# Optimization experiments

Measured on AMD Instinct MI355X. Metric: run time of the kernel, lower is better.

## Reference

```python
import jax, jax.numpy as jnp
import numpy as np

T, B, I, H = 8192, 1, 1024, 1024


def _lstm_layer(x, W_ih, W_hh, b_ih, b_hh):
    # x: [T, B, I]; torch gate order: input, forget, cell(g), output
    Hh = W_hh.shape[1]
    xg = jnp.einsum('tbi,gi->tbg', x, W_ih) + b_ih + b_hh  # [T, B, 4H]

    def step(carry, xg_t):
        h, c = carry
        gates = xg_t + h @ W_hh.T  # [B, 4H]
        i, f, g, o = jnp.split(gates, 4, axis=-1)
        c = jax.nn.sigmoid(f) * c + jax.nn.sigmoid(i) * jnp.tanh(g)
        h = jax.nn.sigmoid(o) * jnp.tanh(c)
        return (h, c), h

    h0 = jnp.zeros((x.shape[1], Hh), x.dtype)
    (_, _), ys = jax.lax.scan(step, (h0, h0), xg)
    return ys  # [T, B, H]


def setup_inputs() -> dict:
    key = jax.random.key(0)
    ks = jax.random.split(key, 9)
    s = 0.02
    return {
        'inputs': jax.random.normal(ks[0], (T, B, I), dtype=jnp.float32),
        'W_ih0': jax.random.normal(ks[1], (4 * H, I), dtype=jnp.float32) * s,
        'W_hh0': jax.random.normal(ks[2], (4 * H, H), dtype=jnp.float32) * s,
        'b_ih0': jax.random.normal(ks[3], (4 * H,), dtype=jnp.float32) * s,
        'b_hh0': jax.random.normal(ks[4], (4 * H,), dtype=jnp.float32) * s,
        'W_ih1': jax.random.normal(ks[5], (4 * H, H), dtype=jnp.float32) * s,
        'W_hh1': jax.random.normal(ks[6], (4 * H, H), dtype=jnp.float32) * s,
        'b_ih1': jax.random.normal(ks[7], (4 * H,), dtype=jnp.float32) * s,
        'b_hh1': jax.random.normal(ks[8], (4 * H,), dtype=jnp.float32) * s,
    }


def reference(inputs, W_ih0, W_hh0, b_ih0, b_hh0, W_ih1, W_hh1, b_ih1, b_hh1):
    # 2-layer LSTM, zero initial state, dropout omitted (eval semantics)
    y0 = _lstm_layer(inputs, W_ih0, W_hh0, b_ih0, b_hh0)
    y1 = _lstm_layer(y0, W_ih1, W_hh1, b_ih1, b_hh1)
    return y1[-1]  # [B, H] — last timestep of top layer
```

## Files before the change

kernel.cpp:

```cpp
#include <hip/hip_runtime.h>

#define T_STEPS 8192
#define HID 1024
#define G4 4096
#define NBLK 128
#define NTHR 512
#define NSLOT 8

typedef unsigned int uint32;

struct Comm {
    uint32 hA[NSLOT][HID];
    uint32 hB[NSLOT][HID];
};

#define LD_AG  __HIP_MEMORY_SCOPE_AGENT

__device__ inline float sigm(float x) { return 1.0f / (1.0f + __expf(-x)); }
__device__ inline float tanh_f(float x) {
    x = fminf(fmaxf(x, -15.f), 15.f);
    float e = __expf(-2.0f * x);
    return (1.0f - e) / (1.0f + e);
}
__device__ inline uint32 tagf(float f, uint32 tg) {
    union { float f; uint32 u; } a; a.f = f;
    return (a.u & ~15u) | tg;
}

__global__ __launch_bounds__(256)
void gemm_xg(const float* __restrict__ A, const float* __restrict__ W,
             const float* __restrict__ bi, const float* __restrict__ bh,
             float* __restrict__ out)
{
    __shared__ float As[16][65];
    __shared__ float Bs[16][65];
    const int tid = threadIdx.x;
    const int m0 = blockIdx.y * 64, n0 = blockIdx.x * 64;
    const int tm = tid & 15, tn = tid >> 4;
    const int row = tid >> 2, q = tid & 3;
    float acc[4][4] = {{0.f}};
    for (int k0 = 0; k0 < HID; k0 += 16) {
        float4 a = *(const float4*)(A + (size_t)(m0 + row) * HID + k0 + q * 4);
        float4 b = *(const float4*)(W + (size_t)(n0 + row) * HID + k0 + q * 4);
        __syncthreads();
        As[q*4+0][row] = a.x; As[q*4+1][row] = a.y; As[q*4+2][row] = a.z; As[q*4+3][row] = a.w;
        Bs[q*4+0][row] = b.x; Bs[q*4+1][row] = b.y; Bs[q*4+2][row] = b.z; Bs[q*4+3][row] = b.w;
        __syncthreads();
#pragma unroll
        for (int kk = 0; kk < 16; ++kk) {
            float av[4], bv[4];
#pragma unroll
            for (int i = 0; i < 4; ++i) { av[i] = As[kk][tm*4+i]; bv[i] = Bs[kk][tn*4+i]; }
#pragma unroll
            for (int i = 0; i < 4; ++i)
#pragma unroll
                for (int j = 0; j < 4; ++j) acc[i][j] += av[i] * bv[j];
        }
    }
#pragma unroll
    for (int i = 0; i < 4; ++i) {
        int m = m0 + tm * 4 + i;
#pragma unroll
        for (int j = 0; j < 4; ++j) {
            int n = n0 + tn * 4 + j;
            float v = acc[i][j] + bi[n] + bh[n];
            int jd = n & (HID - 1), gate = n >> 10;
            out[(size_t)m * G4 + (jd >> 3) * 32 + (jd & 7) * 4 + gate] = v;
        }
    }
}

__device__ __forceinline__ void red4(float& a0, float& a1, float& a2, float& a3)
{
#pragma unroll
    for (int off = 32; off > 0; off >>= 1) {
        a0 += __shfl_xor(a0, off, 64);
        a1 += __shfl_xor(a1, off, 64);
        a2 += __shfl_xor(a2, off, 64);
        a3 += __shfl_xor(a3, off, 64);
    }
}

__device__ __forceinline__ void poll_gather(const uint32* __restrict__ buf, uint32 tg,
                                            int lane, float* __restrict__ lds)
{
    const uint32* p = buf + lane * 4;
    uint4 v0, v1, v2, v3;
    unsigned done = 0;
    for (;;) {
        if (!(done & 1u)) asm volatile("global_load_dwordx4 %0, %1, off sc0 sc1"             : "=v"(v0) : "v"(p) : "memory");
        if (!(done & 2u)) asm volatile("global_load_dwordx4 %0, %1, off offset:1024 sc0 sc1" : "=v"(v1) : "v"(p) : "memory");
        if (!(done & 4u)) asm volatile("global_load_dwordx4 %0, %1, off offset:2048 sc0 sc1" : "=v"(v2) : "v"(p) : "memory");
        if (!(done & 8u)) asm volatile("global_load_dwordx4 %0, %1, off offset:3072 sc0 sc1" : "=v"(v3) : "v"(p) : "memory");
        asm volatile("s_waitcnt vmcnt(0)" ::: "memory");
        __builtin_amdgcn_sched_barrier(0);
        if (!(done & 1u) && (v0.x & 15u) == tg && (v0.y & 15u) == tg &&
            (v0.z & 15u) == tg && (v0.w & 15u) == tg) done |= 1u;
        if (!(done & 2u) && (v1.x & 15u) == tg && (v1.y & 15u) == tg &&
            (v1.z & 15u) == tg && (v1.w & 15u) == tg) done |= 2u;
        if (!(done & 4u) && (v2.x & 15u) == tg && (v2.y & 15u) == tg &&
            (v2.z & 15u) == tg && (v2.w & 15u) == tg) done |= 4u;
        if (!(done & 8u) && (v3.x & 15u) == tg && (v3.y & 15u) == tg &&
            (v3.z & 15u) == tg && (v3.w & 15u) == tg) done |= 8u;
        if (__all(done == 15u)) break;
        __builtin_amdgcn_s_sleep(1);
    }
    union { uint4 u; float4 f; } c;
    c.u = v0; ((float4*)lds)[  0 + lane] = c.f;
    c.u = v1; ((float4*)lds)[ 64 + lane] = c.f;
    c.u = v2; ((float4*)lds)[128 + lane] = c.f;
    c.u = v3; ((float4*)lds)[192 + lane] = c.f;
}

__global__ __launch_bounds__(NTHR)
void lstm_fused(const float* __restrict__ Whh0, const float* __restrict__ xg,
                const float* __restrict__ Wih1, const float* __restrict__ Whh1,
                const float* __restrict__ bih1, const float* __restrict__ bhh1,
                float* __restrict__ outF, Comm* __restrict__ cm)
{
    __shared__ float hlA[2][HID];
    __shared__ float hlB[2][HID];
    const int tid = threadIdx.x;
    const int wave = tid >> 6, lane = tid & 63;
    const int kb = blockIdx.x;
    const int j = 8 * kb + wave;

    float whh0[4][16], whh1[4][16], wih1[4][16];
#pragma unroll
    for (int g = 0; g < 4; ++g) {
        const float* p0 = Whh0 + (size_t)(g * HID + j) * HID + lane;
        const float* p1 = Whh1 + (size_t)(g * HID + j) * HID + lane;
        const float* p2 = Wih1 + (size_t)(g * HID + j) * HID + lane;
#pragma unroll
        for (int u = 0; u < 16; ++u) {
            whh0[g][u] = p0[u * 64];
            whh1[g][u] = p1[u * 64];
            wih1[g][u] = p2[u * 64];
        }
    }
    float bia[4];
#pragma unroll
    for (int g = 0; g < 4; ++g) bia[g] = bih1[g * HID + j] + bhh1[g * HID + j];

    for (int i = tid; i < HID; i += NTHR) {
        hlA[0][i] = 0.f; hlA[1][i] = 0.f; hlB[0][i] = 0.f; hlB[1][i] = 0.f;
    }

    float c0 = 0.f, c1 = 0.f;
    float nx0 = 0.f, nx1 = 0.f, nx2 = 0.f, nx3 = 0.f;
    if (lane == 0) {
        const float* xp = xg + kb * 32 + wave * 4;
        nx0 = xp[0]; nx1 = xp[1]; nx2 = xp[2]; nx3 = xp[3];
    }
    __syncthreads();

    for (int t = 0; t < T_STEPS; ++t) {
        const int p = t & 1;
        const float* hA = hlA[p];
        const float* hB = hlB[p];
        float x0 = nx0, x1 = nx1, x2 = nx2, x3 = nx3;
        if (lane == 0 && t + 1 < T_STEPS) {
            const float* xp = xg + (size_t)(t + 1) * G4 + kb * 32 + wave * 4;
            nx0 = xp[0]; nx1 = xp[1]; nx2 = xp[2]; nx3 = xp[3];
        }
        float a0 = 0.f, a1 = 0.f, a2 = 0.f, a3 = 0.f;
#pragma unroll
        for (int u = 0; u < 16; ++u) {
            float hv = hA[u * 64 + lane];
            a0 += whh0[0][u] * hv; a1 += whh0[1][u] * hv;
            a2 += whh0[2][u] * hv; a3 += whh0[3][u] * hv;
        }
        red4(a0, a1, a2, a3);
        if (lane == 0) {
            float ig = sigm(x0 + a0), fg = sigm(x1 + a1);
            float gg = tanh_f(x2 + a2), og = sigm(x3 + a3);
            c0 = fg * c0 + ig * gg;
            float h = og * tanh_f(c0);
            __hip_atomic_store(&cm->hA[t & 7][j], tagf(h, (t >> 3) & 15),
                               __ATOMIC_RELAXED, LD_AG);
        }
        if (t >= 1) {
            float b0 = 0.f, b1 = 0.f, b2 = 0.f, b3 = 0.f;
#pragma unroll
            for (int u = 0; u < 16; ++u) {
                float h0v = hA[u * 64 + lane];
                float h1v = hB[u * 64 + lane];
                b0 += whh1[0][u] * h1v + wih1[0][u] * h0v;
                b1 += whh1[1][u] * h1v + wih1[1][u] * h0v;
                b2 += whh1[2][u] * h1v + wih1[2][u] * h0v;
                b3 += whh1[3][u] * h1v + wih1[3][u] * h0v;
            }
            red4(b0, b1, b2, b3);
            if (lane == 0) {
                float ig = sigm(bia[0] + b0), fg = sigm(bia[1] + b1);
                float gg = tanh_f(bia[2] + b2), og = sigm(bia[3] + b3);
                c1 = fg * c1 + ig * gg;
                float h = og * tanh_f(c1);
                __hip_atomic_store(&cm->hB[(t - 1) & 7][j],
                                   tagf(h, ((t - 1) >> 3) & 15),
                                   __ATOMIC_RELAXED, LD_AG);
            }
        }
        if (wave == 0) {
            poll_gather((const uint32*)cm->hA[t & 7], (uint32)((t >> 3) & 15),
                        lane, hlA[p ^ 1]);
        } else if (wave == 1 && t >= 1) {
            poll_gather((const uint32*)cm->hB[(t - 1) & 7],
                        (uint32)(((t - 1) >> 3) & 15), lane, hlB[p ^ 1]);
        }
        __syncthreads();
    }
    {
        const float* hA = hlA[T_STEPS & 1];
        const float* hB = hlB[T_STEPS & 1];
        float b0 = 0.f, b1 = 0.f, b2 = 0.f, b3 = 0.f;
#pragma unroll
        for (int u = 0; u < 16; ++u) {
            float h0v = hA[u * 64 + lane];
            float h1v = hB[u * 64 + lane];
            b0 += whh1[0][u] * h1v + wih1[0][u] * h0v;
            b1 += whh1[1][u] * h1v + wih1[1][u] * h0v;
            b2 += whh1[2][u] * h1v + wih1[2][u] * h0v;
            b3 += whh1[3][u] * h1v + wih1[3][u] * h0v;
        }
        red4(b0, b1, b2, b3);
        if (lane == 0) {
            float ig = sigm(bia[0] + b0), fg = sigm(bia[1] + b1);
            float gg = tanh_f(bia[2] + b2), og = sigm(bia[3] + b3);
            c1 = fg * c1 + ig * gg;
            outF[j] = og * tanh_f(c1);
        }
    }
}

extern "C" void kernel_launch(void* const* d_in, const int* in_sizes, int n_in,
                              void* d_out, int out_size, void* d_ws, size_t ws_size,
                              hipStream_t stream)
{
    const float* x    = (const float*)d_in[0];
    const float* Wih0 = (const float*)d_in[1];
    const float* Whh0 = (const float*)d_in[2];
    const float* bih0 = (const float*)d_in[3];
    const float* bhh0 = (const float*)d_in[4];
    const float* Wih1 = (const float*)d_in[5];
    const float* Whh1 = (const float*)d_in[6];
    const float* bih1 = (const float*)d_in[7];
    const float* bhh1 = (const float*)d_in[8];

    char* ws = (char*)d_ws;
    float* xg = (float*)ws;
    Comm*  cm = (Comm*)(ws + 134217728);

    (void)hipMemsetAsync(ws + 134217728, 0xFF, sizeof(Comm), stream);

    dim3 gg(G4 / 64, T_STEPS / 64);
    gemm_xg<<<gg, 256, 0, stream>>>(x, Wih0, bih0, bhh0, xg);
    lstm_fused<<<NBLK, NTHR, 0, stream>>>(Whh0, xg, Wih1, Whh1, bih1, bhh1,
                                          (float*)d_out, cm);
}
```

Measured before the change: 42.40 ms.

## Split LSTM into XCD-specialized layer groups with pipelined input projection blocks

The single fused recurrent kernel is replaced by 256 blocks that specialise by XCD index. One XCD group runs the layer-0 recurrence, another runs the layer-1 recurrence, and four more compute the layer-1 input projection W_ih1·h0 one step ahead, passing it through a tagged ring buffer. Each recurrent block keeps its W_hh slice in registers plus LDS. Blocks publish h both to a same-XCD mirror polled with sc0 loads and to the agent-scope buffer, falling back to the latter after a retry cap. The aim is to take W_ih1 work off layer 1's critical path and cut cross-XCD polling latency. The cost is more complex flow control, with back-pressure spins and a reliance on the hardware mapping blocks to XCDs round-robin.

Result: slower. 52.38 ms (+23.5%).

```diff
diff --git a/kernel.cpp b/kernel.cpp
--- a/kernel.cpp
+++ b/kernel.cpp
@@ -3,28 +3,58 @@
 #define T_STEPS 8192
 #define HID 1024
 #define G4 4096
-#define NBLK 128
 #define NTHR 512
-#define NSLOT 8
 
 typedef unsigned int uint32;
 
-struct Comm {
-    uint32 hA[NSLOT][HID];
-    uint32 hB[NSLOT][HID];
-};
-
-#define LD_AG  __HIP_MEMORY_SCOPE_AGENT
-
-__device__ inline float sigm(float x) { return 1.0f / (1.0f + __expf(-x)); }
-__device__ inline float tanh_f(float x) {
-    x = fminf(fmaxf(x, -15.f), 15.f);
-    float e = __expf(-2.0f * x);
-    return (1.0f - e) / (1.0f + e);
-}
-__device__ inline uint32 tagf(float f, uint32 tg) {
-    union { float f; uint32 u; } a; a.f = f;
-    return (a.u & ~15u) | tg;
+
+__device__ inline float sigm(float x){ return 1.0f/(1.0f+__expf(-x)); }
+__device__ inline float tanh_f(float x){
+    x = fminf(fmaxf(x,-15.f),15.f);
+    float e = __expf(-2.0f*x);
+    return (1.0f-e)/(1.0f+e);
+}
+__device__ inline uint32 tagf(float f, uint32 tg){
+    union{float f;uint32 u;}a; a.f=f; return (a.u & ~15u)|tg;
+}
+__device__ inline float u2f(uint32 u){ union{uint32 u;float f;}a; a.u=u; return a.f; }
+
+__device__ __forceinline__ void pub(uint32* p, uint32 v){
+    __hip_atomic_store(p, v, __ATOMIC_RELAXED, __HIP_MEMORY_SCOPE_AGENT);
+}
+__device__ __forceinline__ void stmir(uint32* p, uint32 v){
+    asm volatile("global_store_dword %0, %1, off" :: "v"(p), "v"(v) : "memory");
+}
+__device__ __forceinline__ uint2 ld2_mir(const uint32* p){
+    uint2 v;
+    asm volatile("global_load_dwordx2 %0, %1, off sc0\ns_waitcnt vmcnt(0)"
+                 : "=v"(v) : "v"(p) : "memory");
+    __builtin_amdgcn_sched_barrier(0);
+    return v;
+}
+__device__ __forceinline__ uint2 ld2_llc(const uint32* p){
+    uint2 v;
+    asm volatile("global_load_dwordx2 %0, %1, off sc0 sc1\ns_waitcnt vmcnt(0)"
+                 : "=v"(v) : "v"(p) : "memory");
+    __builtin_amdgcn_sched_barrier(0);
+    return v;
+}
+__device__ __forceinline__ uint4 ld4_llc(const uint32* p){
+    uint4 v;
+    asm volatile("global_load_dwordx4 %0, %1, off sc0 sc1\ns_waitcnt vmcnt(0)"
+                 : "=v"(v) : "v"(p) : "memory");
+    __builtin_amdgcn_sched_barrier(0);
+    return v;
+}
+__device__ __forceinline__ void issue4(uint4& r, const uint32* p){
+    asm volatile("global_load_dwordx4 %0, %1, off sc0 sc1" : "=v"(r) : "v"(p) : "memory");
+}
+__device__ __forceinline__ uint32 ld1_llc(const uint32* p){
+    uint32 v;
+    asm volatile("global_load_dword %0, %1, off sc0 sc1\ns_waitcnt vmcnt(0)"
+                 : "=v"(v) : "v"(p) : "memory");
+    __builtin_amdgcn_sched_barrier(0);
+    return v;
 }
 
 __global__ __launch_bounds__(256)
@@ -65,170 +95,200 @@
             int n = n0 + tn * 4 + j;
             float v = acc[i][j] + bi[n] + bh[n];
             int jd = n & (HID - 1), gate = n >> 10;
-            out[(size_t)m * G4 + (jd >> 3) * 32 + (jd & 7) * 4 + gate] = v;
+            out[(size_t)m * G4 + jd * 4 + gate] = v;
         }
     }
-}
-
-__device__ __forceinline__ void red4(float& a0, float& a1, float& a2, float& a3)
-{
-#pragma unroll
-    for (int off = 32; off > 0; off >>= 1) {
-        a0 += __shfl_xor(a0, off, 64);
-        a1 += __shfl_xor(a1, off, 64);
-        a2 += __shfl_xor(a2, off, 64);
-        a3 += __shfl_xor(a3, off, 64);
-    }
-}
-
-__device__ __forceinline__ void poll_gather(const uint32* __restrict__ buf, uint32 tg,
-                                            int lane, float* __restrict__ lds)
-{
-    const uint32* p = buf + lane * 4;
-    uint4 v0, v1, v2, v3;
-    unsigned done = 0;
-    for (;;) {
-        if (!(done & 1u)) asm volatile("global_load_dwordx4 %0, %1, off sc0 sc1"             : "=v"(v0) : "v"(p) : "memory");
-        if (!(done & 2u)) asm volatile("global_load_dwordx4 %0, %1, off offset:1024 sc0 sc1" : "=v"(v1) : "v"(p) : "memory");
-        if (!(done & 4u)) asm volatile("global_load_dwordx4 %0, %1, off offset:2048 sc0 sc1" : "=v"(v2) : "v"(p) : "memory");
-        if (!(done & 8u)) asm volatile("global_load_dwordx4 %0, %1, off offset:3072 sc0 sc1" : "=v"(v3) : "v"(p) : "memory");
-        asm volatile("s_waitcnt vmcnt(0)" ::: "memory");
-        __builtin_amdgcn_sched_barrier(0);
-        if (!(done & 1u) && (v0.x & 15u) == tg && (v0.y & 15u) == tg &&
-            (v0.z & 15u) == tg && (v0.w & 15u) == tg) done |= 1u;
-        if (!(done & 2u) && (v1.x & 15u) == tg && (v1.y & 15u) == tg &&
-            (v1.z & 15u) == tg && (v1.w & 15u) == tg) done |= 2u;
-        if (!(done & 4u) && (v2.x & 15u) == tg && (v2.y & 15u) == tg &&
-            (v2.z & 15u) == tg && (v2.w & 15u) == tg) done |= 4u;
-        if (!(done & 8u) && (v3.x & 15u) == tg && (v3.y & 15u) == tg &&
-            (v3.z & 15u) == tg && (v3.w & 15u) == tg) done |= 8u;
-        if (__all(done == 15u)) break;
-        __builtin_amdgcn_s_sleep(1);
-    }
-    union { uint4 u; float4 f; } c;
-    c.u = v0; ((float4*)lds)[  0 + lane] = c.f;
-    c.u = v1; ((float4*)lds)[ 64 + lane] = c.f;
-    c.u = v2; ((float4*)lds)[128 + lane] = c.f;
-    c.u = v3; ((float4*)lds)[192 + lane] = c.f;
 }
 
 __global__ __launch_bounds__(NTHR)
 void lstm_fused(const float* __restrict__ Whh0, const float* __restrict__ xg,
                 const float* __restrict__ Wih1, const float* __restrict__ Whh1,
                 const float* __restrict__ bih1, const float* __restrict__ bhh1,
-                float* __restrict__ outF, Comm* __restrict__ cm)
+                float* __restrict__ outF,
+                uint32* __restrict__ hA, uint32* __restrict__ hB,
+                uint32* __restrict__ zB, uint32* __restrict__ m0,
+                uint32* __restrict__ m1)
 {
-    __shared__ float hlA[2][HID];
-    __shared__ float hlB[2][HID];
-    const int tid = threadIdx.x;
+    __shared__ float4 wlds4[16][512];
+    __shared__ __align__(16) float hl[2][1024];
+
+    const int b = blockIdx.x, tid = threadIdx.x;
+    const int xcd = b & 7, sl = b >> 3;
     const int wave = tid >> 6, lane = tid & 63;
-    const int kb = blockIdx.x;
-    const int j = 8 * kb + wave;
-
-    float whh0[4][16], whh1[4][16], wih1[4][16];
-#pragma unroll
-    for (int g = 0; g < 4; ++g) {
-        const float* p0 = Whh0 + (size_t)(g * HID + j) * HID + lane;
-        const float* p1 = Whh1 + (size_t)(g * HID + j) * HID + lane;
-        const float* p2 = Wih1 + (size_t)(g * HID + j) * HID + lane;
-#pragma unroll
-        for (int u = 0; u < 16; ++u) {
-            whh0[g][u] = p0[u * 64];
-            whh1[g][u] = p1[u * 64];
-            wih1[g][u] = p2[u * 64];
+    if (xcd >= 6) return;
+
+    if (xcd < 2) {
+        const bool isL1 = (xcd == 1);
+        const float* W = isL1 ? Whh1 : Whh0;
+        uint32* mir = isL1 ? m1 : m0;
+        uint32* gho = isL1 ? hB : hA;
+        const int q = lane >> 4;
+        const int row = wave * 16 + (lane & 15);
+        const int grow = (row & 3) * HID + sl * 32 + (row >> 2);
+        const float* wr = W + (size_t)grow * HID;
+        float4 wv[48];
+#pragma unroll
+        for (int e = 0; e < 48; ++e)
+            wv[e] = *(const float4*)(wr + 4 * (q * 64 + ((e + q) & 63)));
+#pragma unroll
+        for (int k = 0; k < 16; ++k)
+            wlds4[k][tid] = *(const float4*)(wr + 4 * (q * 64 + ((48 + k + q) & 63)));
+        for (int i = tid; i < HID; i += NTHR) hl[0][i] = 0.f;
+
+        const int xoff = sl * 128 + wave * 16 + (lane & 12);
+        float4 xv;
+        float4 xnx;
+        uint4  znx;
+        if (!isL1) xnx = *(const float4*)(xg + xoff);
+        else       issue4(znx, zB + xoff);
+        float c = 0.f;
+        bool useLLC = false;
+        __syncthreads();
+
+        for (int t = 0; ; ++t) {
+            const float* hp = hl[t & 1];
+            float a0 = 0.f, a1 = 0.f;
+#pragma unroll
+            for (int e = 0; e < 48; ++e) {
+                const float4 h4 = *(const float4*)(hp + 4 * (q * 64 + ((e + q) & 63)));
+                a0 += wv[e].x * h4.x + wv[e].y * h4.y;
+                a1 += wv[e].z * h4.z + wv[e].w * h4.w;
+            }
+#pragma unroll
+            for (int k = 0; k < 16; ++k) {
+                const float4 wk = wlds4[k][tid];
+                const float4 h4 = *(const float4*)(hp + 4 * (q * 64 + ((48 + k + q) & 63)));
+                a0 += wk.x * h4.x + wk.y * h4.y;
+                a1 += wk.z * h4.z + wk.w * h4.w;
+            }
+            float s = a0 + a1;
+            s += __shfl_xor(s, 16, 64);
+            s += __shfl_xor(s, 32, 64);
+            const int base = lane & 60;
+            float si = __shfl(s, base + 0, 64);
+            float sf = __shfl(s, base + 1, 64);
+            float sg = __shfl(s, base + 2, 64);
+            float so = __shfl(s, base + 3, 64);
+            if (isL1) {
+                asm volatile("s_waitcnt vmcnt(0)" ::: "memory");
+                __builtin_amdgcn_sched_barrier(0);
+                const uint32 ztg = (uint32)((t >> 3) & 15);
+                if (!__all(((znx.x & 15u) == ztg) & ((znx.y & 15u) == ztg) &
+                           ((znx.z & 15u) == ztg) & ((znx.w & 15u) == ztg))) {
+                    const uint32* p = zB + (size_t)(t & 7) * G4 + xoff;
+                    for (;;) {
+                        znx = ld4_llc(p);
+                        if (__all(((znx.x & 15u) == ztg) & ((znx.y & 15u) == ztg) &
+                                  ((znx.z & 15u) == ztg) & ((znx.w & 15u) == ztg))) break;
+                    }
+                }
+                xv.x = u2f(znx.x); xv.y = u2f(znx.y); xv.z = u2f(znx.z); xv.w = u2f(znx.w);
+            } else {
+                xv = xnx;
+            }
+            float ig = sigm(xv.x + si);
+            float fg = sigm(xv.y + sf);
+            float gg = tanh_f(xv.z + sg);
+            float og = sigm(xv.w + so);
+            c = fg * c + ig * gg;
+            float h = og * tanh_f(c);
+
+            const int slot = t & 7;
+            const uint32 tg = (uint32)((t >> 3) & 15);
+            if (isL1 && t == T_STEPS - 1) {
+                if ((lane & 3) == 0 && q == 0)
+                    outF[sl * 32 + wave * 4 + (lane >> 2)] = h;
+                break;
+            }
+            if ((lane & 3) == 0 && q == 0) {
+                const int j = sl * 32 + wave * 4 + (lane >> 2);
+                const uint32 tv = tagf(h, tg);
+                stmir(mir + slot * HID + j, tv);
+                pub(gho + slot * HID + j, tv);
+            }
+            if (t == T_STEPS - 1) break;
+            {
+                float* dst = hl[(t + 1) & 1] + wave * 128 + lane * 2;
+                const uint32* pm = mir + slot * HID + wave * 128 + lane * 2;
+                const uint32* pl = gho + slot * HID + wave * 128 + lane * 2;
+                int it = 0; const int cap = (t == 0) ? 4096 : 256;
+                for (;;) {
+                    uint2 v = useLLC ? ld2_llc(pl) : ld2_mir(pm);
+                    if (__all(((v.x & 15u) == tg) & ((v.y & 15u) == tg))) {
+                        dst[0] = u2f(v.x); dst[1] = u2f(v.y); break;
+                    }
+                    if (!useLLC && ++it >= cap) useLLC = true;
+                }
+            }
+            if (isL1) {
+                if (t + 1 < T_STEPS)
+                    issue4(znx, zB + (size_t)((t + 1) & 7) * G4 + xoff);
+            } else if (t + 1 < T_STEPS) {
+                xnx = *(const float4*)(xg + (size_t)(t + 1) * G4 + xoff);
+            }
+            if (!isL1 && wave == 7 && (t & 3) == 0 && t >= 4) {
+                {
+                    const uint32 stg = (uint32)(((t - 4) >> 3) & 15);
+                    const uint32* p = zB + (size_t)((t - 4) & 7) * G4 + lane * 64;
+                    for (;;) { if (__all((ld1_llc(p) & 15u) == stg)) break; }
+                }
+                if (t >= 8) {
+                    const uint32 stg = (uint32)(((t - 5) >> 3) & 15);
+                    const uint32* p = zB + (size_t)((t - 5) & 7) * G4 + lane * 64;
+                    for (;;) { if (__all((ld1_llc(p) & 15u) == stg)) break; }
+                }
+            }
+            __syncthreads();
         }
-    }
-    float bia[4];
-#pragma unroll
-    for (int g = 0; g < 4; ++g) bia[g] = bih1[g * HID + j] + bhh1[g * HID + j];
-
-    for (int i = tid; i < HID; i += NTHR) {
-        hlA[0][i] = 0.f; hlA[1][i] = 0.f; hlB[0][i] = 0.f; hlB[1][i] = 0.f;
-    }
-
-    float c0 = 0.f, c1 = 0.f;
-    float nx0 = 0.f, nx1 = 0.f, nx2 = 0.f, nx3 = 0.f;
-    if (lane == 0) {
-        const float* xp = xg + kb * 32 + wave * 4;
-        nx0 = xp[0]; nx1 = xp[1]; nx2 = xp[2]; nx3 = xp[3];
-    }
-    __syncthreads();
-
-    for (int t = 0; t < T_STEPS; ++t) {
-        const int p = t & 1;
-        const float* hA = hlA[p];
-        const float* hB = hlB[p];
-        float x0 = nx0, x1 = nx1, x2 = nx2, x3 = nx3;
-        if (lane == 0 && t + 1 < T_STEPS) {
-            const float* xp = xg + (size_t)(t + 1) * G4 + kb * 32 + wave * 4;
-            nx0 = xp[0]; nx1 = xp[1]; nx2 = xp[2]; nx3 = xp[3];
-        }
-        float a0 = 0.f, a1 = 0.f, a2 = 0.f, a3 = 0.f;
-#pragma unroll
-        for (int u = 0; u < 16; ++u) {
-            float hv = hA[u * 64 + lane];
-            a0 += whh0[0][u] * hv; a1 += whh0[1][u] * hv;
-            a2 += whh0[2][u] * hv; a3 += whh0[3][u] * hv;
-        }
-        red4(a0, a1, a2, a3);
-        if (lane == 0) {
-            float ig = sigm(x0 + a0), fg = sigm(x1 + a1);
-            float gg = tanh_f(x2 + a2), og = sigm(x3 + a3);
-            c0 = fg * c0 + ig * gg;
-            float h = og * tanh_f(c0);
-            __hip_atomic_store(&cm->hA[t & 7][j], tagf(h, (t >> 3) & 15),
-                               __ATOMIC_RELAXED, LD_AG);
-        }
-        if (t >= 1) {
-            float b0 = 0.f, b1 = 0.f, b2 = 0.f, b3 = 0.f;
-#pragma unroll
-            for (int u = 0; u < 16; ++u) {
-                float h0v = hA[u * 64 + lane];
-                float h1v = hB[u * 64 + lane];
-                b0 += whh1[0][u] * h1v + wih1[0][u] * h0v;
-                b1 += whh1[1][u] * h1v + wih1[1][u] * h0v;
-                b2 += whh1[2][u] * h1v + wih1[2][u] * h0v;
-                b3 += whh1[3][u] * h1v + wih1[3][u] * h0v;
-            }
-            red4(b0, b1, b2, b3);
-            if (lane == 0) {
-                float ig = sigm(bia[0] + b0), fg = sigm(bia[1] + b1);
-                float gg = tanh_f(bia[2] + b2), og = sigm(bia[3] + b3);
-                c1 = fg * c1 + ig * gg;
-                float h = og * tanh_f(c1);
-                __hip_atomic_store(&cm->hB[(t - 1) & 7][j],
-                                   tagf(h, ((t - 1) >> 3) & 15),
-                                   __ATOMIC_RELAXED, LD_AG);
-            }
-        }
-        if (wave == 0) {
-            poll_gather((const uint32*)cm->hA[t & 7], (uint32)((t >> 3) & 15),
-                        lane, hlA[p ^ 1]);
-        } else if (wave == 1 && t >= 1) {
-            poll_gather((const uint32*)cm->hB[(t - 1) & 7],
-                        (uint32)(((t - 1) >> 3) & 15), lane, hlB[p ^ 1]);
-        }
+    } else {
+        const int f = (xcd - 2) * 32 + sl;
+        const int ph = f & 1, kp = f >> 1;
+        const int q8 = lane >> 3;
+        const int row = wave * 8 + (lane & 7);
+        const int grow = (row & 3) * HID + kp * 16 + (row >> 2);
+        const float* wr = Wih1 + (size_t)grow * HID;
+        float4 wf[32];
+#pragma unroll
+        for (int e = 0; e < 32; ++e)
+            wf[e] = *(const float4*)(wr + 4 * (q8 * 32 + ((e + q8) & 31)));
+        const float bia = bih1[grow] + bhh1[grow];
         __syncthreads();
-    }
-    {
-        const float* hA = hlA[T_STEPS & 1];
-        const float* hB = hlB[T_STEPS & 1];
-        float b0 = 0.f, b1 = 0.f, b2 = 0.f, b3 = 0.f;
-#pragma unroll
-        for (int u = 0; u < 16; ++u) {
-            float h0v = hA[u * 64 + lane];
-            float h1v = hB[u * 64 + lane];
-            b0 += whh1[0][u] * h1v + wih1[0][u] * h0v;
-            b1 += whh1[1][u] * h1v + wih1[1][u] * h0v;
-            b2 += whh1[2][u] * h1v + wih1[2][u] * h0v;
-            b3 += whh1[3][u] * h1v + wih1[3][u] * h0v;
-        }
-        red4(b0, b1, b2, b3);
-        if (lane == 0) {
-            float ig = sigm(bia[0] + b0), fg = sigm(bia[1] + b1);
-            float gg = tanh_f(bia[2] + b2), og = sigm(bia[3] + b3);
-            c1 = fg * c1 + ig * gg;
-            outF[j] = og * tanh_f(c1);
+
+        for (int u = ph; u < T_STEPS; u += 2) {
+            const int slot = u & 7;
+            const uint32 tg = (uint32)((u >> 3) & 15);
+            {
+                const uint32* p = hA + slot * HID + tid * 2;
+                uint2 v;
+                for (;;) {
+                    v = ld2_llc(p);
+                    if (__all(((v.x & 15u) == tg) & ((v.y & 15u) == tg))) break;
+                }
+                float* hb = hl[(u >> 1) & 1];
+                hb[tid * 2] = u2f(v.x); hb[tid * 2 + 1] = u2f(v.y);
+            }
+            if (wave == 0 && ((u >> 1) & 1) == 0 && u >= 4) {
+                const uint32 stg = (uint32)(((u - 4) >> 3) & 15);
+                const uint32* p = hB + (size_t)((u - 4) & 7) * HID + (lane & 31) * 32;
+                for (;;) { if (__all((ld1_llc(p) & 15u) == stg)) break; }
+            }
+            __syncthreads();
+            const float* hp = hl[(u >> 1) & 1];
+            float a0 = 0.f, a1 = 0.f;
+#pragma unroll
+            for (int e = 0; e < 32; ++e) {
+                const float4 h4 = *(const float4*)(hp + 4 * (q8 * 32 + ((e + q8) & 31)));
+                a0 += wf[e].x * h4.x + wf[e].y * h4.y;
+                a1 += wf[e].z * h4.z + wf[e].w * h4.w;
+            }
+            float s = a0 + a1;
+            s += __shfl_xor(s, 8, 64);
+            s += __shfl_xor(s, 16, 64);
+            s += __shfl_xor(s, 32, 64);
+            if (lane < 8) {
+                const int zi = (kp * 16 + wave * 2 + (lane >> 2)) * 4 + (lane & 3);
+                pub(zB + (size_t)slot * G4 + zi, tagf(s + bia, tg));
+            }
         }
     }
 }
@@ -249,12 +309,17 @@
 
     char* ws = (char*)d_ws;
     float* xg = (float*)ws;
-    Comm*  cm = (Comm*)(ws + 134217728);
-
-    (void)hipMemsetAsync(ws + 134217728, 0xFF, sizeof(Comm), stream);
+    size_t off = 134217728ull;
+    uint32* hA = (uint32*)(ws + off); off += 32768;
+    uint32* hB = (uint32*)(ws + off); off += 32768;
+    uint32* m0 = (uint32*)(ws + off); off += 32768;
+    uint32* m1 = (uint32*)(ws + off); off += 32768;
+    uint32* zB = (uint32*)(ws + off); off += 131072;
+
+    (void)hipMemsetAsync(ws + 134217728ull, 0xFF, 262144, stream);
 
     dim3 gg(G4 / 64, T_STEPS / 64);
     gemm_xg<<<gg, 256, 0, stream>>>(x, Wih0, bih0, bhh0, xg);
-    lstm_fused<<<NBLK, NTHR, 0, stream>>>(Whh0, xg, Wih1, Whh1, bih1, bhh1,
-                                          (float*)d_out, cm);
-}
+    lstm_fused<<<256, NTHR, 0, stream>>>(Whh0, xg, Wih1, Whh1, bih1, bhh1,
+                                         (float*)d_out, hA, hB, zB, m0, m1);
+}
```
